# Kernel tuning notes

Measured on AMD Instinct MI355X. Metric: run time of the kernel, lower is better.

## Reference

```python
import jax, jax.numpy as jnp
import numpy as np

B = 8192
N = 722          # number of independent tiny MLPs
CAM = 10         # CAMERA_VECTOR_DIM
IN = CAM + 1     # per-MLP input dim
H = 10           # hidden dim
LOD = 6          # NUM_LOD_LEVELS


def setup_inputs() -> dict:
    key = jax.random.key(0)
    ks = jax.random.split(key, 8)
    return {
        "prior_lod": jax.random.uniform(ks[0], (B, N), dtype=jnp.float32),
        "camera": jax.random.normal(ks[1], (B, CAM), dtype=jnp.float32),
        "W1": jax.random.normal(ks[2], (N, IN, H), dtype=jnp.float32) * 0.3,
        "b1": jax.random.normal(ks[3], (N, H), dtype=jnp.float32) * 0.1,
        "W2": jax.random.normal(ks[4], (N, H, H), dtype=jnp.float32) * 0.3,
        "b2": jax.random.normal(ks[5], (N, H), dtype=jnp.float32) * 0.1,
        "W3": jax.random.normal(ks[6], (N, H, LOD), dtype=jnp.float32) * 0.3,
        "b3": jax.random.normal(ks[7], (N, LOD), dtype=jnp.float32) * 0.1,
    }


def reference(prior_lod, camera, W1, b1, W2, b2, W3, b3):
    # Per-network input: cat(prior_lod[:, i:i+1], camera) -> [B, N, IN]
    cam = jnp.broadcast_to(camera[:, None, :], (prior_lod.shape[0], W1.shape[0], camera.shape[1]))
    x = jnp.concatenate([prior_lod[:, :, None], cam], axis=-1)  # [B, N, IN]
    # Batched 3-layer MLP over the N axis (grouped GEMM equivalent of the 722-loop)
    h = jax.nn.relu(jnp.einsum('bni,nih->bnh', x, W1) + b1[None])   # [B, N, H]
    h = jax.nn.relu(jnp.einsum('bnh,nhk->bnk', h, W2) + b2[None])   # [B, N, H]
    out = jnp.einsum('bnh,nho->bno', h, W3) + b3[None]              # [B, N, LOD]
    return out  # stacked version of the original list of 722 [B, LOD] outputs
```

## Files before the change

### kernel.cpp

```cpp
#include <hip/hip_runtime.h>


#define NN 722
#define CAMD 10
#define HD 10
#define LODD 6
#define ROWF (NN * LODD)
#define BT 256
#define NETS_PER_CHUNK 4
#define NCHUNKS 181
#define CPG 2
#define NGROUPS 91
#define LSTRIDE 25
#define HROWS 128

#define NETSTRIDE 368
#define OFF_W2 132
#define OFF_W3 252
#define OFF_B1 332
#define OFF_B2 344
#define OFF_B3 356

__device__ __forceinline__ void lds_barrier() {
    asm volatile("s_waitcnt lgkmcnt(0)" ::: "memory");
    __builtin_amdgcn_s_barrier();
}

#define LOAD10(dst, base) do {                                   \
    const float4 _a = *(const float4*)(base);                    \
    const float4 _b = *(const float4*)((base) + 4);              \
    const float2 _c = *(const float2*)((base) + 8);              \
    dst[0]=_a.x; dst[1]=_a.y; dst[2]=_a.z; dst[3]=_a.w;          \
    dst[4]=_b.x; dst[5]=_b.y; dst[6]=_b.z; dst[7]=_b.w;          \
    dst[8]=_c.x; dst[9]=_c.y; } while (0)

#define LOAD6(dst, base) do {                                    \
    const float4 _a = *(const float4*)(base);                    \
    const float2 _c = *(const float2*)((base) + 4);              \
    dst[0]=_a.x; dst[1]=_a.y; dst[2]=_a.z; dst[3]=_a.w;          \
    dst[4]=_c.x; dst[5]=_c.y; } while (0)

__global__ __launch_bounds__(256, 4) void Net_18966575579675_kernel(
    const float* __restrict__ prior, const float* __restrict__ camera,
    const float* __restrict__ W1, const float* __restrict__ b1,
    const float* __restrict__ W2, const float* __restrict__ b2,
    const float* __restrict__ W3, const float* __restrict__ b3,
    float* __restrict__ out)
{
    const int tid  = threadIdx.x;
    const int lane = tid & 63;
    const int wave = __builtin_amdgcn_readfirstlane(tid >> 6);
    const int b0   = blockIdx.x * BT;

    const int c_begin = blockIdx.y * CPG;
    const int c_end   = (c_begin + CPG < NCHUNKS) ? (c_begin + CPG) : NCHUNKS;

    __shared__ float2 cam2[CAMD / 2][BT];
    __shared__ float  obuf[HROWS * LSTRIDE];
    __shared__ __align__(16) float wbuf[2][NETS_PER_CHUNK * NETSTRIDE];

    {
        const float2* c2 = (const float2*)(camera + (size_t)(b0 + tid) * CAMD);
#pragma unroll
        for (int i = 0; i < CAMD / 2; ++i)
            cam2[i][tid] = c2[i];
    }

    auto stage_now = [&](int cc) {
        const int ns = cc * NETS_PER_CHUNK + wave;
        if (ns < NN) {
            float* wd = &wbuf[cc & 1][wave * NETSTRIDE];
            const float* s1 = W1 + (size_t)ns * (CAMD + 1) * HD;
#pragma unroll
            for (int t0 = 0; t0 < 110; t0 += 64) {
                const int t = t0 + lane;
                if (t < 110) { const int i = t / 10, j = t - 10 * i; wd[i * 12 + j] = s1[t]; }
            }
            const float* s2 = W2 + (size_t)ns * HD * HD;
#pragma unroll
            for (int t0 = 0; t0 < 100; t0 += 64) {
                const int t = t0 + lane;
                if (t < 100) { const int j = t / 10, k = t - 10 * j; wd[OFF_W2 + j * 12 + k] = s2[t]; }
            }
            const float* s3 = W3 + (size_t)ns * HD * LODD;
            if (lane < 60) { const int j = lane / 6, m = lane - 6 * j; wd[OFF_W3 + j * 8 + m] = s3[lane]; }
            if (lane < 10)      wd[OFF_B1 + lane]      = b1[(size_t)ns * HD + lane];
            else if (lane < 20) wd[OFF_B2 + lane - 10] = b2[(size_t)ns * HD + lane - 10];
            else if (lane < 26) wd[OFF_B3 + lane - 20] = b3[(size_t)ns * LODD + lane - 20];
        }
    };

    stage_now(c_begin);

    float pr0, pr1, pr2, pr3;
    {
        const int n0 = c_begin * NETS_PER_CHUNK + wave;
        const int nc = n0 < NN ? n0 : NN - 1;
        pr0 = prior[(size_t)(b0 + 0 * 64 + lane) * NN + nc];
        pr1 = prior[(size_t)(b0 + 1 * 64 + lane) * NN + nc];
        pr2 = prior[(size_t)(b0 + 2 * 64 + lane) * NN + nc];
        pr3 = prior[(size_t)(b0 + 3 * 64 + lane) * NN + nc];
    }

    lds_barrier();

#pragma unroll 1
    for (int c = c_begin; c < c_end; ++c) {
        const int n   = c * NETS_PER_CHUNK + wave;
        const bool act = (n < NN);

        if (c + 1 < c_end) stage_now(c + 1);

        float nx0 = pr0, nx1 = pr1, nx2 = pr2, nx3 = pr3;
        if (c + 1 < c_end) {
            const int n1 = (c + 1) * NETS_PER_CHUNK + wave;
            const int nc = n1 < NN ? n1 : NN - 1;
            nx0 = prior[(size_t)(b0 + 0 * 64 + lane) * NN + nc];
            nx1 = prior[(size_t)(b0 + 1 * 64 + lane) * NN + nc];
            nx2 = prior[(size_t)(b0 + 2 * 64 + lane) * NN + nc];
            nx3 = prior[(size_t)(b0 + 3 * 64 + lane) * NN + nc];
        }

        float o[4][LODD];
        if (act) {
            const float* wb = &wbuf[c & 1][wave * NETSTRIDE];

            float h1[4][HD];
            {
                float bv[10]; LOAD10(bv, wb + OFF_B1);
                float wv[10]; LOAD10(wv, wb);
#pragma unroll
                for (int j = 0; j < HD; ++j) {
                    h1[0][j] = fmaf(pr0, wv[j], bv[j]);
                    h1[1][j] = fmaf(pr1, wv[j], bv[j]);
                    h1[2][j] = fmaf(pr2, wv[j], bv[j]);
                    h1[3][j] = fmaf(pr3, wv[j], bv[j]);
                }
            }
#pragma unroll
            for (int i2 = 0; i2 < CAMD / 2; ++i2) {
                const float2 c0 = cam2[i2][0 * 64 + lane];
                const float2 c1 = cam2[i2][1 * 64 + lane];
                const float2 c2v = cam2[i2][2 * 64 + lane];
                const float2 c3 = cam2[i2][3 * 64 + lane];
                float wa[10]; LOAD10(wa, wb + (2 * i2 + 1) * 12);
                float wc[10]; LOAD10(wc, wb + (2 * i2 + 2) * 12);
#pragma unroll
                for (int j = 0; j < HD; ++j) {
                    h1[0][j] = fmaf(c0.x, wa[j], h1[0][j]);
                    h1[1][j] = fmaf(c1.x, wa[j], h1[1][j]);
                    h1[2][j] = fmaf(c2v.x, wa[j], h1[2][j]);
                    h1[3][j] = fmaf(c3.x, wa[j], h1[3][j]);
                }
#pragma unroll
                for (int j = 0; j < HD; ++j) {
                    h1[0][j] = fmaf(c0.y, wc[j], h1[0][j]);
                    h1[1][j] = fmaf(c1.y, wc[j], h1[1][j]);
                    h1[2][j] = fmaf(c2v.y, wc[j], h1[2][j]);
                    h1[3][j] = fmaf(c3.y, wc[j], h1[3][j]);
                }
            }
#pragma unroll
            for (int s = 0; s < 4; ++s)
#pragma unroll
                for (int j = 0; j < HD; ++j)
                    h1[s][j] = fmaxf(h1[s][j], 0.0f);

            float h2[4][HD];
            {
                float bv[10]; LOAD10(bv, wb + OFF_B2);
#pragma unroll
                for (int k = 0; k < HD; ++k) {
                    h2[0][k] = bv[k]; h2[1][k] = bv[k];
                    h2[2][k] = bv[k]; h2[3][k] = bv[k];
                }
            }
#pragma unroll
            for (int j = 0; j < HD; ++j) {
                float wv[10]; LOAD10(wv, wb + OFF_W2 + j * 12);
#pragma unroll
                for (int k = 0; k < HD; ++k) {
                    h2[0][k] = fmaf(h1[0][j], wv[k], h2[0][k]);
                    h2[1][k] = fmaf(h1[1][j], wv[k], h2[1][k]);
                    h2[2][k] = fmaf(h1[2][j], wv[k], h2[2][k]);
                    h2[3][k] = fmaf(h1[3][j], wv[k], h2[3][k]);
                }
            }
#pragma unroll
            for (int s = 0; s < 4; ++s)
#pragma unroll
                for (int k = 0; k < HD; ++k)
                    h2[s][k] = fmaxf(h2[s][k], 0.0f);

            {
                float bv[6]; LOAD6(bv, wb + OFF_B3);
#pragma unroll
                for (int m = 0; m < LODD; ++m) {
                    o[0][m] = bv[m]; o[1][m] = bv[m];
                    o[2][m] = bv[m]; o[3][m] = bv[m];
                }
            }
#pragma unroll
            for (int j = 0; j < HD; ++j) {
                float wv[6]; LOAD6(wv, wb + OFF_W3 + j * 8);
#pragma unroll
                for (int m = 0; m < LODD; ++m) {
                    o[0][m] = fmaf(h2[0][j], wv[m], o[0][m]);
                    o[1][m] = fmaf(h2[1][j], wv[m], o[1][m]);
                    o[2][m] = fmaf(h2[2][j], wv[m], o[2][m]);
                    o[3][m] = fmaf(h2[3][j], wv[m], o[3][m]);
                }
            }
        }

        const int rem = NN - c * NETS_PER_CHUNK;
        const int nv  = rem < NETS_PER_CHUNK ? rem : NETS_PER_CHUNK;

#pragma unroll
        for (int h = 0; h < 2; ++h) {
            if (act) {
#pragma unroll
                for (int ss = 0; ss < 2; ++ss) {
                    const int s = 2 * h + ss;
#pragma unroll
                    for (int m = 0; m < LODD; ++m)
                        obuf[(ss * 64 + lane) * LSTRIDE + wave * LODD + m] =
                            (s == 0) ? o[0][m] : (s == 1) ? o[1][m]
                          : (s == 2) ? o[2][m] : o[3][m];
                }
            }
            lds_barrier();

            if (nv == NETS_PER_CHUNK) {
                for (int f = tid; f < HROWS * 6; f += 256) {
                    const int row  = f / 6;
                    const int colq = f - row * 6;
                    const float* sp = obuf + row * LSTRIDE + colq * 4;
                    float4 v = make_float4(sp[0], sp[1], sp[2], sp[3]);
                    *(float4*)(out + (size_t)(b0 + h * HROWS + row) * ROWF
                               + c * (NETS_PER_CHUNK * LODD) + colq * 4) = v;
                }
            } else {
                for (int f = tid; f < HROWS * 3; f += 256) {
                    const int row  = f / 3;
                    const int colq = f - row * 3;
                    const float* sp = obuf + row * LSTRIDE + colq * 4;
                    float4 v = make_float4(sp[0], sp[1], sp[2], sp[3]);
                    *(float4*)(out + (size_t)(b0 + h * HROWS + row) * ROWF
                               + c * (NETS_PER_CHUNK * LODD) + colq * 4) = v;
                }
            }
            lds_barrier();
        }

        pr0 = nx0; pr1 = nx1; pr2 = nx2; pr3 = nx3;
    }
}

extern "C" void kernel_launch(void* const* d_in, const int* in_sizes, int n_in,
                              void* d_out, int out_size, void* d_ws, size_t ws_size,
                              hipStream_t stream) {
    const float* prior  = (const float*)d_in[0];
    const float* camera = (const float*)d_in[1];
    const float* W1     = (const float*)d_in[2];
    const float* b1     = (const float*)d_in[3];
    const float* W2     = (const float*)d_in[4];
    const float* b2     = (const float*)d_in[5];
    const float* W3     = (const float*)d_in[6];
    const float* b3     = (const float*)d_in[7];
    float* out = (float*)d_out;

    dim3 grid(8192 / BT, NGROUPS);
    dim3 block(256);
    Net_18966575579675_kernel<<<grid, block, 0, stream>>>(
        prior, camera, W1, b1, W2, b2, W3, b3, out);
}
```

Baseline: 242.0 us.

## Stage 16 nets per block and write wider coalesced output rows

Each block now stages the weights of 16 nets (4 chunks) into LDS up front instead of double-buffering 2 chunks, and the grid shrinks from 91 to 46 groups. Samples are processed in two halves of 128 rows with 2 rows per lane. Camera values are held in registers rather than LDS. Output is written as 96-float-wide row segments, so global stores are wider and more contiguous. In exchange, the weight load is no longer overlapped with compute, occupancy is lowered to 3 blocks per CU, and more barriers are needed per output tile.

```diff
diff --git a/kernel.cpp b/kernel.cpp
--- a/kernel.cpp
+++ b/kernel.cpp
@@ -6,13 +6,9 @@
 #define HD 10
 #define LODD 6
 #define ROWF (NN * LODD)
-#define BT 256
-#define NETS_PER_CHUNK 4
 #define NCHUNKS 181
-#define CPG 2
-#define NGROUPS 91
-#define LSTRIDE 25
-#define HROWS 128
+#define NG 46
+#define OSTRIDE 97
 
 #define NETSTRIDE 368
 #define OFF_W2 132
@@ -40,7 +36,7 @@
     dst[0]=_a.x; dst[1]=_a.y; dst[2]=_a.z; dst[3]=_a.w;          \
     dst[4]=_c.x; dst[5]=_c.y; } while (0)
 
-__global__ __launch_bounds__(256, 4) void Net_18966575579675_kernel(
+__global__ __launch_bounds__(256, 3) void Net_18966575579675_kernel(
     const float* __restrict__ prior, const float* __restrict__ camera,
     const float* __restrict__ W1, const float* __restrict__ b1,
     const float* __restrict__ W2, const float* __restrict__ b2,
@@ -50,210 +46,220 @@
     const int tid  = threadIdx.x;
     const int lane = tid & 63;
     const int wave = __builtin_amdgcn_readfirstlane(tid >> 6);
-    const int b0   = blockIdx.x * BT;
-
-    const int c_begin = blockIdx.y * CPG;
-    const int c_end   = (c_begin + CPG < NCHUNKS) ? (c_begin + CPG) : NCHUNKS;
-
-    __shared__ float2 cam2[CAMD / 2][BT];
-    __shared__ float  obuf[HROWS * LSTRIDE];
-    __shared__ __align__(16) float wbuf[2][NETS_PER_CHUNK * NETSTRIDE];
-
+    const int b0   = blockIdx.x * 256;
+    const int g    = blockIdx.y;
+    const int cig  = (g == NG - 1) ? 1 : 4;
+
+    __shared__ __align__(16) float wbuf[16 * NETSTRIDE];
+    __shared__ float obuf[64 * OSTRIDE];
+
+#pragma unroll
+    for (int c = 0; c < 4; ++c) {
+        if (c < cig) {
+            const int ns = g * 16 + c * 4 + wave;
+            if (ns < NN) {
+                float* wd = wbuf + (c * 4 + wave) * NETSTRIDE;
+                const float* s1 = W1 + (size_t)ns * (CAMD + 1) * HD;
+#pragma unroll
+                for (int t0 = 0; t0 < 110; t0 += 64) {
+                    const int t = t0 + lane;
+                    if (t < 110) { const int i = t / 10, j = t - 10 * i; wd[i * 12 + j] = s1[t]; }
+                }
+                const float* s2 = W2 + (size_t)ns * HD * HD;
+#pragma unroll
+                for (int t0 = 0; t0 < 100; t0 += 64) {
+                    const int t = t0 + lane;
+                    if (t < 100) { const int j = t / 10, k = t - 10 * j; wd[OFF_W2 + j * 12 + k] = s2[t]; }
+                }
+                const float* s3 = W3 + (size_t)ns * HD * LODD;
+                if (lane < 60) { const int j = lane / 6, m = lane - 6 * j; wd[OFF_W3 + j * 8 + m] = s3[lane]; }
+                if (lane < 10)      wd[OFF_B1 + lane]      = b1[(size_t)ns * HD + lane];
+                else if (lane < 20) wd[OFF_B2 + lane - 10] = b2[(size_t)ns * HD + lane - 10];
+                else if (lane < 26) wd[OFF_B3 + lane - 20] = b3[(size_t)ns * LODD + lane - 20];
+            }
+        }
+    }
+
+    float prC0, prC1;
     {
-        const float2* c2 = (const float2*)(camera + (size_t)(b0 + tid) * CAMD);
-#pragma unroll
-        for (int i = 0; i < CAMD / 2; ++i)
-            cam2[i][tid] = c2[i];
+        const int n0 = g * 16 + wave;
+        const int nc = n0 < NN ? n0 : NN - 1;
+        prC0 = prior[(size_t)(b0 + lane) * NN + nc];
+        prC1 = prior[(size_t)(b0 + 64 + lane) * NN + nc];
     }
 
-    auto stage_now = [&](int cc) {
-        const int ns = cc * NETS_PER_CHUNK + wave;
-        if (ns < NN) {
-            float* wd = &wbuf[cc & 1][wave * NETSTRIDE];
-            const float* s1 = W1 + (size_t)ns * (CAMD + 1) * HD;
-#pragma unroll
-            for (int t0 = 0; t0 < 110; t0 += 64) {
-                const int t = t0 + lane;
-                if (t < 110) { const int i = t / 10, j = t - 10 * i; wd[i * 12 + j] = s1[t]; }
-            }
-            const float* s2 = W2 + (size_t)ns * HD * HD;
-#pragma unroll
-            for (int t0 = 0; t0 < 100; t0 += 64) {
-                const int t = t0 + lane;
-                if (t < 100) { const int j = t / 10, k = t - 10 * j; wd[OFF_W2 + j * 12 + k] = s2[t]; }
-            }
-            const float* s3 = W3 + (size_t)ns * HD * LODD;
-            if (lane < 60) { const int j = lane / 6, m = lane - 6 * j; wd[OFF_W3 + j * 8 + m] = s3[lane]; }
-            if (lane < 10)      wd[OFF_B1 + lane]      = b1[(size_t)ns * HD + lane];
-            else if (lane < 20) wd[OFF_B2 + lane - 10] = b2[(size_t)ns * HD + lane - 10];
-            else if (lane < 26) wd[OFF_B3 + lane - 20] = b3[(size_t)ns * LODD + lane - 20];
-        }
-    };
-
-    stage_now(c_begin);
-
-    float pr0, pr1, pr2, pr3;
-    {
-        const int n0 = c_begin * NETS_PER_CHUNK + wave;
-        const int nc = n0 < NN ? n0 : NN - 1;
-        pr0 = prior[(size_t)(b0 + 0 * 64 + lane) * NN + nc];
-        pr1 = prior[(size_t)(b0 + 1 * 64 + lane) * NN + nc];
-        pr2 = prior[(size_t)(b0 + 2 * 64 + lane) * NN + nc];
-        pr3 = prior[(size_t)(b0 + 3 * 64 + lane) * NN + nc];
-    }
-
-    lds_barrier();
-
 #pragma unroll 1
-    for (int c = c_begin; c < c_end; ++c) {
-        const int n   = c * NETS_PER_CHUNK + wave;
-        const bool act = (n < NN);
-
-        if (c + 1 < c_end) stage_now(c + 1);
-
-        float nx0 = pr0, nx1 = pr1, nx2 = pr2, nx3 = pr3;
-        if (c + 1 < c_end) {
-            const int n1 = (c + 1) * NETS_PER_CHUNK + wave;
-            const int nc = n1 < NN ? n1 : NN - 1;
-            nx0 = prior[(size_t)(b0 + 0 * 64 + lane) * NN + nc];
-            nx1 = prior[(size_t)(b0 + 1 * 64 + lane) * NN + nc];
-            nx2 = prior[(size_t)(b0 + 2 * 64 + lane) * NN + nc];
-            nx3 = prior[(size_t)(b0 + 3 * 64 + lane) * NN + nc];
-        }
-
-        float o[4][LODD];
-        if (act) {
-            const float* wb = &wbuf[c & 1][wave * NETSTRIDE];
-
-            float h1[4][HD];
-            {
-                float bv[10]; LOAD10(bv, wb + OFF_B1);
-                float wv[10]; LOAD10(wv, wb);
-#pragma unroll
-                for (int j = 0; j < HD; ++j) {
-                    h1[0][j] = fmaf(pr0, wv[j], bv[j]);
-                    h1[1][j] = fmaf(pr1, wv[j], bv[j]);
-                    h1[2][j] = fmaf(pr2, wv[j], bv[j]);
-                    h1[3][j] = fmaf(pr3, wv[j], bv[j]);
-                }
-            }
-#pragma unroll
-            for (int i2 = 0; i2 < CAMD / 2; ++i2) {
-                const float2 c0 = cam2[i2][0 * 64 + lane];
-                const float2 c1 = cam2[i2][1 * 64 + lane];
-                const float2 c2v = cam2[i2][2 * 64 + lane];
-                const float2 c3 = cam2[i2][3 * 64 + lane];
-                float wa[10]; LOAD10(wa, wb + (2 * i2 + 1) * 12);
-                float wc[10]; LOAD10(wc, wb + (2 * i2 + 2) * 12);
-#pragma unroll
-                for (int j = 0; j < HD; ++j) {
-                    h1[0][j] = fmaf(c0.x, wa[j], h1[0][j]);
-                    h1[1][j] = fmaf(c1.x, wa[j], h1[1][j]);
-                    h1[2][j] = fmaf(c2v.x, wa[j], h1[2][j]);
-                    h1[3][j] = fmaf(c3.x, wa[j], h1[3][j]);
-                }
-#pragma unroll
-                for (int j = 0; j < HD; ++j) {
-                    h1[0][j] = fmaf(c0.y, wc[j], h1[0][j]);
-                    h1[1][j] = fmaf(c1.y, wc[j], h1[1][j]);
-                    h1[2][j] = fmaf(c2v.y, wc[j], h1[2][j]);
-                    h1[3][j] = fmaf(c3.y, wc[j], h1[3][j]);
-                }
-            }
-#pragma unroll
-            for (int s = 0; s < 4; ++s)
-#pragma unroll
-                for (int j = 0; j < HD; ++j)
-                    h1[s][j] = fmaxf(h1[s][j], 0.0f);
-
-            float h2[4][HD];
-            {
-                float bv[10]; LOAD10(bv, wb + OFF_B2);
-#pragma unroll
-                for (int k = 0; k < HD; ++k) {
-                    h2[0][k] = bv[k]; h2[1][k] = bv[k];
-                    h2[2][k] = bv[k]; h2[3][k] = bv[k];
-                }
-            }
-#pragma unroll
-            for (int j = 0; j < HD; ++j) {
-                float wv[10]; LOAD10(wv, wb + OFF_W2 + j * 12);
-#pragma unroll
-                for (int k = 0; k < HD; ++k) {
-                    h2[0][k] = fmaf(h1[0][j], wv[k], h2[0][k]);
-                    h2[1][k] = fmaf(h1[1][j], wv[k], h2[1][k]);
-                    h2[2][k] = fmaf(h1[2][j], wv[k], h2[2][k]);
-                    h2[3][k] = fmaf(h1[3][j], wv[k], h2[3][k]);
-                }
-            }
-#pragma unroll
-            for (int s = 0; s < 4; ++s)
-#pragma unroll
-                for (int k = 0; k < HD; ++k)
-                    h2[s][k] = fmaxf(h2[s][k], 0.0f);
-
-            {
-                float bv[6]; LOAD6(bv, wb + OFF_B3);
-#pragma unroll
-                for (int m = 0; m < LODD; ++m) {
-                    o[0][m] = bv[m]; o[1][m] = bv[m];
-                    o[2][m] = bv[m]; o[3][m] = bv[m];
-                }
-            }
-#pragma unroll
-            for (int j = 0; j < HD; ++j) {
-                float wv[6]; LOAD6(wv, wb + OFF_W3 + j * 8);
-#pragma unroll
-                for (int m = 0; m < LODD; ++m) {
-                    o[0][m] = fmaf(h2[0][j], wv[m], o[0][m]);
-                    o[1][m] = fmaf(h2[1][j], wv[m], o[1][m]);
-                    o[2][m] = fmaf(h2[2][j], wv[m], o[2][m]);
-                    o[3][m] = fmaf(h2[3][j], wv[m], o[3][m]);
-                }
-            }
-        }
-
-        const int rem = NN - c * NETS_PER_CHUNK;
-        const int nv  = rem < NETS_PER_CHUNK ? rem : NETS_PER_CHUNK;
-
-#pragma unroll
-        for (int h = 0; h < 2; ++h) {
-            if (act) {
-#pragma unroll
-                for (int ss = 0; ss < 2; ++ss) {
-                    const int s = 2 * h + ss;
+    for (int q = 0; q < 2; ++q) {
+        float camA[CAMD], camB[CAMD];
+        {
+            const float2* ca = (const float2*)(camera + (size_t)(b0 + q * 128 + lane) * CAMD);
+            const float2* cb = (const float2*)(camera + (size_t)(b0 + q * 128 + 64 + lane) * CAMD);
+#pragma unroll
+            for (int i = 0; i < CAMD / 2; ++i) {
+                const float2 va = ca[i];
+                const float2 vb = cb[i];
+                camA[2 * i] = va.x; camA[2 * i + 1] = va.y;
+                camB[2 * i] = vb.x; camB[2 * i + 1] = vb.y;
+            }
+        }
+
+        float o2[4][LODD];
+
+#pragma unroll
+        for (int c = 0; c < 4; ++c) {
+            if (c < cig) {
+                const int n   = g * 16 + c * 4 + wave;
+                const bool act = (n < NN);
+
+                float nx0 = prC0, nx1 = prC1;
+                {
+                    int nq = q, nc = c + 1;
+                    bool have = true;
+                    if (nc >= cig) { nc = 0; nq = q + 1; have = (nq < 2); }
+                    if (have) {
+                        const int nn2 = g * 16 + nc * 4 + wave;
+                        const int nnc = nn2 < NN ? nn2 : NN - 1;
+                        nx0 = prior[(size_t)(b0 + nq * 128 + lane) * NN + nnc];
+                        nx1 = prior[(size_t)(b0 + nq * 128 + 64 + lane) * NN + nnc];
+                    }
+                }
+
+                if (act) {
+                    const float* wb = wbuf + (c * 4 + wave) * NETSTRIDE;
+
+                    float h1[2][HD];
+                    {
+                        float bv[10]; LOAD10(bv, wb + OFF_B1);
+                        float wv[10]; LOAD10(wv, wb);
+#pragma unroll
+                        for (int j = 0; j < HD; ++j) {
+                            h1[0][j] = fmaf(prC0, wv[j], bv[j]);
+                            h1[1][j] = fmaf(prC1, wv[j], bv[j]);
+                        }
+                    }
+#pragma unroll
+                    for (int i2 = 0; i2 < CAMD / 2; ++i2) {
+                        float wa[10]; LOAD10(wa, wb + (2 * i2 + 1) * 12);
+                        float wc[10]; LOAD10(wc, wb + (2 * i2 + 2) * 12);
+#pragma unroll
+                        for (int j = 0; j < HD; ++j) {
+                            h1[0][j] = fmaf(camA[2 * i2], wa[j], h1[0][j]);
+                            h1[1][j] = fmaf(camB[2 * i2], wa[j], h1[1][j]);
+                        }
+#pragma unroll
+                        for (int j = 0; j < HD; ++j) {
+                            h1[0][j] = fmaf(camA[2 * i2 + 1], wc[j], h1[0][j]);
+                            h1[1][j] = fmaf(camB[2 * i2 + 1], wc[j], h1[1][j]);
+                        }
+                    }
+#pragma unroll
+                    for (int j = 0; j < HD; ++j) {
+                        h1[0][j] = fmaxf(h1[0][j], 0.0f);
+                        h1[1][j] = fmaxf(h1[1][j], 0.0f);
+                    }
+
+                    float h2[2][HD];
+                    {
+                        float bv[10]; LOAD10(bv, wb + OFF_B2);
+#pragma unroll
+                        for (int k = 0; k < HD; ++k) { h2[0][k] = bv[k]; h2[1][k] = bv[k]; }
+                    }
+#pragma unroll
+                    for (int j = 0; j < HD; ++j) {
+                        float wv[10]; LOAD10(wv, wb + OFF_W2 + j * 12);
+#pragma unroll
+                        for (int k = 0; k < HD; ++k) {
+                            h2[0][k] = fmaf(h1[0][j], wv[k], h2[0][k]);
+                            h2[1][k] = fmaf(h1[1][j], wv[k], h2[1][k]);
+                        }
+                    }
+#pragma unroll
+                    for (int k = 0; k < HD; ++k) {
+                        h2[0][k] = fmaxf(h2[0][k], 0.0f);
+                        h2[1][k] = fmaxf(h2[1][k], 0.0f);
+                    }
+
+                    float o[2][LODD];
+                    {
+                        float bv[6]; LOAD6(bv, wb + OFF_B3);
+#pragma unroll
+                        for (int m = 0; m < LODD; ++m) { o[0][m] = bv[m]; o[1][m] = bv[m]; }
+                    }
+#pragma unroll
+                    for (int j = 0; j < HD; ++j) {
+                        float wv[6]; LOAD6(wv, wb + OFF_W3 + j * 8);
+#pragma unroll
+                        for (int m = 0; m < LODD; ++m) {
+                            o[0][m] = fmaf(h2[0][j], wv[m], o[0][m]);
+                            o[1][m] = fmaf(h2[1][j], wv[m], o[1][m]);
+                        }
+                    }
+
+#pragma unroll
+                    for (int m = 0; m < LODD; ++m) {
+                        obuf[lane * OSTRIDE + c * 24 + wave * LODD + m] = o[0][m];
+                        o2[c][m] = o[1][m];
+                    }
+                }
+                prC0 = nx0; prC1 = nx1;
+            }
+        }
+
+        lds_barrier();
+        if (g < NG - 1) {
+            for (int f = tid; f < 64 * 24; f += 256) {
+                const int row  = f / 24;
+                const int colq = f - row * 24;
+                const float* sp = obuf + row * OSTRIDE + colq * 4;
+                float4 v = make_float4(sp[0], sp[1], sp[2], sp[3]);
+                *(float4*)(out + (size_t)(b0 + q * 128 + row) * ROWF
+                           + g * 96 + colq * 4) = v;
+            }
+        } else {
+            for (int f = tid; f < 64 * 3; f += 256) {
+                const int row  = f / 3;
+                const int colq = f - row * 3;
+                const float* sp = obuf + row * OSTRIDE + colq * 4;
+                float4 v = make_float4(sp[0], sp[1], sp[2], sp[3]);
+                *(float4*)(out + (size_t)(b0 + q * 128 + row) * ROWF
+                           + g * 96 + colq * 4) = v;
+            }
+        }
+        lds_barrier();
+
+#pragma unroll
+        for (int c = 0; c < 4; ++c) {
+            if (c < cig) {
+                const int n = g * 16 + c * 4 + wave;
+                if (n < NN) {
 #pragma unroll
                     for (int m = 0; m < LODD; ++m)
-                        obuf[(ss * 64 + lane) * LSTRIDE + wave * LODD + m] =
-                            (s == 0) ? o[0][m] : (s == 1) ? o[1][m]
-                          : (s == 2) ? o[2][m] : o[3][m];
-                }
-            }
-            lds_barrier();
-
-            if (nv == NETS_PER_CHUNK) {
-                for (int f = tid; f < HROWS * 6; f += 256) {
-                    const int row  = f / 6;
-                    const int colq = f - row * 6;
-                    const float* sp = obuf + row * LSTRIDE + colq * 4;
-                    float4 v = make_float4(sp[0], sp[1], sp[2], sp[3]);
-                    *(float4*)(out + (size_t)(b0 + h * HROWS + row) * ROWF
-                               + c * (NETS_PER_CHUNK * LODD) + colq * 4) = v;
-                }
-            } else {
-                for (int f = tid; f < HROWS * 3; f += 256) {
-                    const int row  = f / 3;
-                    const int colq = f - row * 3;
-                    const float* sp = obuf + row * LSTRIDE + colq * 4;
-                    float4 v = make_float4(sp[0], sp[1], sp[2], sp[3]);
-                    *(float4*)(out + (size_t)(b0 + h * HROWS + row) * ROWF
-                               + c * (NETS_PER_CHUNK * LODD) + colq * 4) = v;
-                }
-            }
-            lds_barrier();
-        }
-
-        pr0 = nx0; pr1 = nx1; pr2 = nx2; pr3 = nx3;
+                        obuf[lane * OSTRIDE + c * 24 + wave * LODD + m] = o2[c][m];
+                }
+            }
+        }
+
+        lds_barrier();
+        if (g < NG - 1) {
+            for (int f = tid; f < 64 * 24; f += 256) {
+                const int row  = f / 24;
+                const int colq = f - row * 24;
+                const float* sp = obuf + row * OSTRIDE + colq * 4;
+                float4 v = make_float4(sp[0], sp[1], sp[2], sp[3]);
+                *(float4*)(out + (size_t)(b0 + q * 128 + 64 + row) * ROWF
+                           + g * 96 + colq * 4) = v;
+            }
+        } else {
+            for (int f = tid; f < 64 * 3; f += 256) {
+                const int row  = f / 3;
+                const int colq = f - row * 3;
+                const float* sp = obuf + row * OSTRIDE + colq * 4;
+                float4 v = make_float4(sp[0], sp[1], sp[2], sp[3]);
+                *(float4*)(out + (size_t)(b0 + q * 128 + 64 + row) * ROWF
+                           + g * 96 + colq * 4) = v;
+            }
+        }
+        lds_barrier();
     }
 }
 
@@ -270,7 +276,7 @@
     const float* b3     = (const float*)d_in[7];
     float* out = (float*)d_out;
 
-    dim3 grid(8192 / BT, NGROUPS);
+    dim3 grid(8192 / 256, NG);
     dim3 block(256);
     Net_18966575579675_kernel<<<grid, block, 0, stream>>>(
         prior, camera, W1, b1, W2, b2, W3, b3, out);
```

Result: faster. 215.4 us (-11.0%).

## Stage all 16 nets per block upfront, keep camera in registers, single-pass output

Applied to the files above, without the earlier changes.

Each block now handles 16 networks (4 chunks) instead of 8. All weights are staged into LDS once at the start, replacing per-chunk double buffering. Camera vectors are held in registers rather than read from LDS, and the output is written in one 256-row pass per chunk instead of two 128-row halves, which halves the barriers. The launch-bounds occupancy hint is dropped. The cost is a larger LDS footprint (weights plus a full obuf) and more registers, which may reduce occupancy, and the grid has half as many blocks.

```diff
diff --git a/kernel.cpp b/kernel.cpp
--- a/kernel.cpp
+++ b/kernel.cpp
@@ -6,13 +6,8 @@
 #define HD 10
 #define LODD 6
 #define ROWF (NN * LODD)
-#define BT 256
-#define NETS_PER_CHUNK 4
-#define NCHUNKS 181
-#define CPG 2
-#define NGROUPS 91
+#define NG 46
 #define LSTRIDE 25
-#define HROWS 128
 
 #define NETSTRIDE 368
 #define OFF_W2 132
@@ -40,7 +35,7 @@
     dst[0]=_a.x; dst[1]=_a.y; dst[2]=_a.z; dst[3]=_a.w;          \
     dst[4]=_c.x; dst[5]=_c.y; } while (0)
 
-__global__ __launch_bounds__(256, 4) void Net_18966575579675_kernel(
+__global__ __launch_bounds__(256) void Net_18966575579675_kernel(
     const float* __restrict__ prior, const float* __restrict__ camera,
     const float* __restrict__ W1, const float* __restrict__ b1,
     const float* __restrict__ W2, const float* __restrict__ b2,
@@ -50,80 +45,79 @@
     const int tid  = threadIdx.x;
     const int lane = tid & 63;
     const int wave = __builtin_amdgcn_readfirstlane(tid >> 6);
-    const int b0   = blockIdx.x * BT;
-
-    const int c_begin = blockIdx.y * CPG;
-    const int c_end   = (c_begin + CPG < NCHUNKS) ? (c_begin + CPG) : NCHUNKS;
-
-    __shared__ float2 cam2[CAMD / 2][BT];
-    __shared__ float  obuf[HROWS * LSTRIDE];
-    __shared__ __align__(16) float wbuf[2][NETS_PER_CHUNK * NETSTRIDE];
-
+    const int b0   = blockIdx.x * 256;
+    const int g    = blockIdx.y;
+    const int cig  = (g == NG - 1) ? 1 : 4;
+
+    __shared__ __align__(16) float wbuf[16 * NETSTRIDE];
+    __shared__ float obuf[256 * LSTRIDE];
+
+#pragma unroll
+    for (int c = 0; c < 4; ++c) {
+        if (c < cig) {
+            const int ns = g * 16 + c * 4 + wave;
+            if (ns < NN) {
+                float* wd = wbuf + (c * 4 + wave) * NETSTRIDE;
+                const float* s1 = W1 + (size_t)ns * (CAMD + 1) * HD;
+#pragma unroll
+                for (int t0 = 0; t0 < 110; t0 += 64) {
+                    const int t = t0 + lane;
+                    if (t < 110) { const int i = t / 10, j = t - 10 * i; wd[i * 12 + j] = s1[t]; }
+                }
+                const float* s2 = W2 + (size_t)ns * HD * HD;
+#pragma unroll
+                for (int t0 = 0; t0 < 100; t0 += 64) {
+                    const int t = t0 + lane;
+                    if (t < 100) { const int j = t / 10, k = t - 10 * j; wd[OFF_W2 + j * 12 + k] = s2[t]; }
+                }
+                const float* s3 = W3 + (size_t)ns * HD * LODD;
+                if (lane < 60) { const int j = lane / 6, m = lane - 6 * j; wd[OFF_W3 + j * 8 + m] = s3[lane]; }
+                if (lane < 10)      wd[OFF_B1 + lane]      = b1[(size_t)ns * HD + lane];
+                else if (lane < 20) wd[OFF_B2 + lane - 10] = b2[(size_t)ns * HD + lane - 10];
+                else if (lane < 26) wd[OFF_B3 + lane - 20] = b3[(size_t)ns * LODD + lane - 20];
+            }
+        }
+    }
+
+    float cam[4][CAMD];
+#pragma unroll
+    for (int s = 0; s < 4; ++s) {
+        const float2* c2 = (const float2*)(camera + (size_t)(b0 + s * 64 + lane) * CAMD);
+#pragma unroll
+        for (int i = 0; i < CAMD / 2; ++i) {
+            const float2 v = c2[i];
+            cam[s][2 * i]     = v.x;
+            cam[s][2 * i + 1] = v.y;
+        }
+    }
+
+    float pr[4];
     {
-        const float2* c2 = (const float2*)(camera + (size_t)(b0 + tid) * CAMD);
-#pragma unroll
-        for (int i = 0; i < CAMD / 2; ++i)
-            cam2[i][tid] = c2[i];
-    }
-
-    auto stage_now = [&](int cc) {
-        const int ns = cc * NETS_PER_CHUNK + wave;
-        if (ns < NN) {
-            float* wd = &wbuf[cc & 1][wave * NETSTRIDE];
-            const float* s1 = W1 + (size_t)ns * (CAMD + 1) * HD;
-#pragma unroll
-            for (int t0 = 0; t0 < 110; t0 += 64) {
-                const int t = t0 + lane;
-                if (t < 110) { const int i = t / 10, j = t - 10 * i; wd[i * 12 + j] = s1[t]; }
-            }
-            const float* s2 = W2 + (size_t)ns * HD * HD;
-#pragma unroll
-            for (int t0 = 0; t0 < 100; t0 += 64) {
-                const int t = t0 + lane;
-                if (t < 100) { const int j = t / 10, k = t - 10 * j; wd[OFF_W2 + j * 12 + k] = s2[t]; }
-            }
-            const float* s3 = W3 + (size_t)ns * HD * LODD;
-            if (lane < 60) { const int j = lane / 6, m = lane - 6 * j; wd[OFF_W3 + j * 8 + m] = s3[lane]; }
-            if (lane < 10)      wd[OFF_B1 + lane]      = b1[(size_t)ns * HD + lane];
-            else if (lane < 20) wd[OFF_B2 + lane - 10] = b2[(size_t)ns * HD + lane - 10];
-            else if (lane < 26) wd[OFF_B3 + lane - 20] = b3[(size_t)ns * LODD + lane - 20];
-        }
-    };
-
-    stage_now(c_begin);
-
-    float pr0, pr1, pr2, pr3;
-    {
-        const int n0 = c_begin * NETS_PER_CHUNK + wave;
+        const int n0 = g * 16 + wave;
         const int nc = n0 < NN ? n0 : NN - 1;
-        pr0 = prior[(size_t)(b0 + 0 * 64 + lane) * NN + nc];
-        pr1 = prior[(size_t)(b0 + 1 * 64 + lane) * NN + nc];
-        pr2 = prior[(size_t)(b0 + 2 * 64 + lane) * NN + nc];
-        pr3 = prior[(size_t)(b0 + 3 * 64 + lane) * NN + nc];
-    }
-
-    lds_barrier();
+#pragma unroll
+        for (int s = 0; s < 4; ++s)
+            pr[s] = prior[(size_t)(b0 + s * 64 + lane) * NN + nc];
+    }
 
 #pragma unroll 1
-    for (int c = c_begin; c < c_end; ++c) {
-        const int n   = c * NETS_PER_CHUNK + wave;
+    for (int c = 0; c < cig; ++c) {
+        const int n   = g * 16 + c * 4 + wave;
         const bool act = (n < NN);
 
-        if (c + 1 < c_end) stage_now(c + 1);
-
-        float nx0 = pr0, nx1 = pr1, nx2 = pr2, nx3 = pr3;
-        if (c + 1 < c_end) {
-            const int n1 = (c + 1) * NETS_PER_CHUNK + wave;
+        float prn[4];
+#pragma unroll
+        for (int s = 0; s < 4; ++s) prn[s] = pr[s];
+        if (c + 1 < cig) {
+            const int n1 = g * 16 + (c + 1) * 4 + wave;
             const int nc = n1 < NN ? n1 : NN - 1;
-            nx0 = prior[(size_t)(b0 + 0 * 64 + lane) * NN + nc];
-            nx1 = prior[(size_t)(b0 + 1 * 64 + lane) * NN + nc];
-            nx2 = prior[(size_t)(b0 + 2 * 64 + lane) * NN + nc];
-            nx3 = prior[(size_t)(b0 + 3 * 64 + lane) * NN + nc];
-        }
-
-        float o[4][LODD];
+#pragma unroll
+            for (int s = 0; s < 4; ++s)
+                prn[s] = prior[(size_t)(b0 + s * 64 + lane) * NN + nc];
+        }
+
         if (act) {
-            const float* wb = &wbuf[c & 1][wave * NETSTRIDE];
+            const float* wb = wbuf + (c * 4 + wave) * NETSTRIDE;
 
             float h1[4][HD];
             {
@@ -131,33 +125,21 @@
                 float wv[10]; LOAD10(wv, wb);
 #pragma unroll
                 for (int j = 0; j < HD; ++j) {
-                    h1[0][j] = fmaf(pr0, wv[j], bv[j]);
-                    h1[1][j] = fmaf(pr1, wv[j], bv[j]);
-                    h1[2][j] = fmaf(pr2, wv[j], bv[j]);
-                    h1[3][j] = fmaf(pr3, wv[j], bv[j]);
-                }
-            }
-#pragma unroll
-            for (int i2 = 0; i2 < CAMD / 2; ++i2) {
-                const float2 c0 = cam2[i2][0 * 64 + lane];
-                const float2 c1 = cam2[i2][1 * 64 + lane];
-                const float2 c2v = cam2[i2][2 * 64 + lane];
-                const float2 c3 = cam2[i2][3 * 64 + lane];
-                float wa[10]; LOAD10(wa, wb + (2 * i2 + 1) * 12);
-                float wc[10]; LOAD10(wc, wb + (2 * i2 + 2) * 12);
+                    h1[0][j] = fmaf(pr[0], wv[j], bv[j]);
+                    h1[1][j] = fmaf(pr[1], wv[j], bv[j]);
+                    h1[2][j] = fmaf(pr[2], wv[j], bv[j]);
+                    h1[3][j] = fmaf(pr[3], wv[j], bv[j]);
+                }
+            }
+#pragma unroll
+            for (int i = 0; i < CAMD; ++i) {
+                float wv[10]; LOAD10(wv, wb + (i + 1) * 12);
 #pragma unroll
                 for (int j = 0; j < HD; ++j) {
-                    h1[0][j] = fmaf(c0.x, wa[j], h1[0][j]);
-                    h1[1][j] = fmaf(c1.x, wa[j], h1[1][j]);
-                    h1[2][j] = fmaf(c2v.x, wa[j], h1[2][j]);
-                    h1[3][j] = fmaf(c3.x, wa[j], h1[3][j]);
-                }
-#pragma unroll
-                for (int j = 0; j < HD; ++j) {
-                    h1[0][j] = fmaf(c0.y, wc[j], h1[0][j]);
-                    h1[1][j] = fmaf(c1.y, wc[j], h1[1][j]);
-                    h1[2][j] = fmaf(c2v.y, wc[j], h1[2][j]);
-                    h1[3][j] = fmaf(c3.y, wc[j], h1[3][j]);
+                    h1[0][j] = fmaf(cam[0][i], wv[j], h1[0][j]);
+                    h1[1][j] = fmaf(cam[1][i], wv[j], h1[1][j]);
+                    h1[2][j] = fmaf(cam[2][i], wv[j], h1[2][j]);
+                    h1[3][j] = fmaf(cam[3][i], wv[j], h1[3][j]);
                 }
             }
 #pragma unroll
@@ -192,6 +174,7 @@
                 for (int k = 0; k < HD; ++k)
                     h2[s][k] = fmaxf(h2[s][k], 0.0f);
 
+            float o[4][LODD];
             {
                 float bv[6]; LOAD6(bv, wb + OFF_B3);
 #pragma unroll
@@ -211,49 +194,40 @@
                     o[3][m] = fmaf(h2[3][j], wv[m], o[3][m]);
                 }
             }
-        }
-
-        const int rem = NN - c * NETS_PER_CHUNK;
-        const int nv  = rem < NETS_PER_CHUNK ? rem : NETS_PER_CHUNK;
-
-#pragma unroll
-        for (int h = 0; h < 2; ++h) {
-            if (act) {
-#pragma unroll
-                for (int ss = 0; ss < 2; ++ss) {
-                    const int s = 2 * h + ss;
-#pragma unroll
-                    for (int m = 0; m < LODD; ++m)
-                        obuf[(ss * 64 + lane) * LSTRIDE + wave * LODD + m] =
-                            (s == 0) ? o[0][m] : (s == 1) ? o[1][m]
-                          : (s == 2) ? o[2][m] : o[3][m];
-                }
-            }
-            lds_barrier();
-
-            if (nv == NETS_PER_CHUNK) {
-                for (int f = tid; f < HROWS * 6; f += 256) {
-                    const int row  = f / 6;
-                    const int colq = f - row * 6;
-                    const float* sp = obuf + row * LSTRIDE + colq * 4;
-                    float4 v = make_float4(sp[0], sp[1], sp[2], sp[3]);
-                    *(float4*)(out + (size_t)(b0 + h * HROWS + row) * ROWF
-                               + c * (NETS_PER_CHUNK * LODD) + colq * 4) = v;
-                }
-            } else {
-                for (int f = tid; f < HROWS * 3; f += 256) {
-                    const int row  = f / 3;
-                    const int colq = f - row * 3;
-                    const float* sp = obuf + row * LSTRIDE + colq * 4;
-                    float4 v = make_float4(sp[0], sp[1], sp[2], sp[3]);
-                    *(float4*)(out + (size_t)(b0 + h * HROWS + row) * ROWF
-                               + c * (NETS_PER_CHUNK * LODD) + colq * 4) = v;
-                }
-            }
-            lds_barrier();
-        }
-
-        pr0 = nx0; pr1 = nx1; pr2 = nx2; pr3 = nx3;
+#pragma unroll
+            for (int s = 0; s < 4; ++s)
+#pragma unroll
+                for (int m = 0; m < LODD; ++m)
+                    obuf[(s * 64 + lane) * LSTRIDE + wave * LODD + m] = o[s][m];
+        }
+
+        lds_barrier();
+
+        const int rem = NN - (g * 16 + c * 4);
+        const int nv  = rem < 4 ? rem : 4;
+        if (nv == 4) {
+            for (int f = tid; f < 256 * 6; f += 256) {
+                const int row  = f / 6;
+                const int colq = f - row * 6;
+                const float* sp = obuf + row * LSTRIDE + colq * 4;
+                float4 v = make_float4(sp[0], sp[1], sp[2], sp[3]);
+                *(float4*)(out + (size_t)(b0 + row) * ROWF
+                           + g * 96 + c * 24 + colq * 4) = v;
+            }
+        } else {
+            for (int f = tid; f < 256 * 3; f += 256) {
+                const int row  = f / 3;
+                const int colq = f - row * 3;
+                const float* sp = obuf + row * LSTRIDE + colq * 4;
+                float4 v = make_float4(sp[0], sp[1], sp[2], sp[3]);
+                *(float4*)(out + (size_t)(b0 + row) * ROWF
+                           + g * 96 + c * 24 + colq * 4) = v;
+            }
+        }
+        lds_barrier();
+
+#pragma unroll
+        for (int s = 0; s < 4; ++s) pr[s] = prn[s];
     }
 }
 
@@ -270,7 +244,7 @@
     const float* b3     = (const float*)d_in[7];
     float* out = (float*)d_out;
 
-    dim3 grid(8192 / BT, NGROUPS);
+    dim3 grid(8192 / 256, NG);
     dim3 block(256);
     Net_18966575579675_kernel<<<grid, block, 0, stream>>>(
         prior, camera, W1, b1, W2, b2, W3, b3, out);
```

After: 255.0 us. 5.4% more time.
